# Performance work log

Measured on AMD Instinct MI355X. Metric: run time of the kernel, lower is better.

Reference implementation:

```python
import jax, jax.numpy as jnp
import numpy as np

NUM_HEADS = 16
N_EMBED = 1024
HEAD_SIZE = 64
BLOCK_SIZE = 2048


def setup_inputs() -> dict:
    key = jax.random.key(0)
    ks = jax.random.split(key, 6)
    B, S, C, H, D = 2, BLOCK_SIZE, N_EMBED, NUM_HEADS, HEAD_SIZE
    x = jax.random.normal(ks[0], (B, S, C), dtype=jnp.float32)
    scale = C ** -0.5
    # per-head q/k/v projections (bias=False), stacked over heads: [H, C, D]
    Wq = jax.random.normal(ks[1], (H, C, D), dtype=jnp.float32) * scale
    Wk = jax.random.normal(ks[2], (H, C, D), dtype=jnp.float32) * scale
    Wv = jax.random.normal(ks[3], (H, C, D), dtype=jnp.float32) * scale
    # output projection Linear(H*D, C)
    Wo = jax.random.normal(ks[4], (H * D, C), dtype=jnp.float32) * ((H * D) ** -0.5)
    bo = jax.random.normal(ks[5], (C,), dtype=jnp.float32) * 0.01
    return {"x": x, "Wq": Wq, "Wk": Wk, "Wv": Wv, "Wo": Wo, "bo": bo}


def reference(x, Wq, Wk, Wv, Wo, bo):
    B, S, C = x.shape
    H, _, D = Wq.shape
    # project: [B, H, S, D]
    q = jnp.einsum("bsc,hcd->bhsd", x, Wq)
    k = jnp.einsum("bsc,hcd->bhsd", x, Wk)
    v = jnp.einsum("bsc,hcd->bhsd", x, Wv)
    # scaled causal attention scores: [B, H, S, S]
    scores = jnp.einsum("bhsd,bhtd->bhst", q, k) * (D ** -0.5)
    causal = jnp.tril(jnp.ones((S, S), dtype=bool))
    scores = jnp.where(causal, scores, jnp.finfo(scores.dtype).min)
    attn = jax.nn.softmax(scores, axis=-1)
    out = jnp.einsum("bhst,bhtd->bhsd", attn, v)  # [B, H, S, D]
    # concat heads -> [B, S, H*D], then output projection
    out = out.transpose(0, 2, 1, 3).reshape(B, S, H * D)
    return out @ Wo + bo
```

## Files before the change

kernel.cpp:

```cpp
#include <hip/hip_runtime.h>
#include <cstdint>
#include <cstddef>

constexpr int SEQ  = 2048;
constexpr int CH   = 1024;
constexpr int NH   = 16;
constexpr int HS   = 64;
constexpr int NB   = 2;
constexpr int HDIM = NH * HS;

typedef __bf16 bf16x8 __attribute__((ext_vector_type(8)));
typedef __bf16 bf16x4 __attribute__((ext_vector_type(4)));
typedef float  f32x4  __attribute__((ext_vector_type(4)));

__device__ __forceinline__ unsigned short f2bf(float f) {
  union { float f; unsigned u; } v; v.f = f;
  unsigned u = v.u;
  u += 0x7fffu + ((u >> 16) & 1u);
  return (unsigned short)(u >> 16);
}
__device__ __forceinline__ float bf2f(unsigned short h) {
  union { unsigned u; float f; } v; v.u = ((unsigned)h) << 16;
  return v.f;
}
__device__ __forceinline__ float load_elem(const void* p, int flag, size_t idx) {
  if (flag) return ((const float*)p)[idx];
  return bf2f(((const unsigned short*)p)[idx]);
}
__device__ __forceinline__ void gl_lds16(const unsigned short* g, unsigned short* l) {
  __builtin_amdgcn_global_load_lds(
      (const __attribute__((address_space(1))) unsigned int*)g,
      (__attribute__((address_space(3))) unsigned int*)l, 16, 0, 0);
}

__device__ int detect_flag_block(const void* p, int n, int tid, int nthr) {
  __shared__ int det_good;
  if (tid == 0) det_good = 0;
  __syncthreads();
  const unsigned short* u = (const unsigned short*)p;
  int good = 0;
  for (int j = tid; j < n; j += nthr) {
    unsigned short v = u[2 * j];
    int e = (v >> 7) & 0xFF;
    if (v != 0 && e >= 90 && e <= 150) good++;
  }
  atomicAdd(&det_good, good);
  __syncthreads();
  return (det_good * 10 >= n * 7) ? 0 : 1;
}

__global__ __launch_bounds__(256) void prep(
    const void* __restrict__ x,  const void* __restrict__ wq,
    const void* __restrict__ wk, const void* __restrict__ wv,
    const void* __restrict__ wo,
    unsigned short* __restrict__ xb,
    unsigned short* __restrict__ wall,
    unsigned short* __restrict__ wot) {
  __shared__ unsigned short tile[32][36];
  int idx = blockIdx.x, tid = threadIdx.x;
  int row = tid >> 3, cg = (tid & 7) * 4;
  int col = tid >> 3, rg = (tid & 7) * 4;
  if (idx < 1024) {
    int f = detect_flag_block(x, 512, tid, 256);
    size_t n4 = (size_t)NB * SEQ * CH / 4;
    for (size_t i = (size_t)idx * 256 + tid; i < n4; i += (size_t)1024 * 256) {
      ushort4 o;
      if (f) {
        float4 v = ((const float4*)x)[i];
        o.x = f2bf(v.x); o.y = f2bf(v.y); o.z = f2bf(v.z); o.w = f2bf(v.w);
      } else {
        o = ((const ushort4*)x)[i];
      }
      ((ushort4*)xb)[i] = o;
    }
  } else if (idx < 4096) {
    int j = idx - 1024;
    int which = j >> 10, hh = (j >> 6) & 15, sub = j & 63;
    const void* src = (which == 0) ? wq : (which == 1) ? wk : wv;
    int f = detect_flag_block(src, 512, tid, 256);
    int c0 = (sub & 1) * 32;
    int r0 = (sub >> 1) * 32;
    size_t boff = (size_t)hh * CH * HS;
    size_t si = boff + (size_t)(r0 + row) * HS + c0 + cg;
    ushort4 t4;
    if (f) {
      float4 v = *(const float4*)((const float*)src + si);
      t4.x = f2bf(v.x); t4.y = f2bf(v.y); t4.z = f2bf(v.z); t4.w = f2bf(v.w);
    } else {
      t4 = *(const ushort4*)((const unsigned short*)src + si);
    }
    *(ushort4*)&tile[row][cg] = t4;
    __syncthreads();
    unsigned short* d = wall + ((size_t)which * NH + hh) * HS * CH;
    ushort4 o;
    o.x = tile[rg + 0][col]; o.y = tile[rg + 1][col];
    o.z = tile[rg + 2][col]; o.w = tile[rg + 3][col];
    *(ushort4*)&d[(size_t)(c0 + col) * CH + r0 + rg] = o;
  } else {
    int sub = idx - 4096;
    int f = detect_flag_block(wo, 512, tid, 256);
    int c0 = (sub & 31) * 32;
    int r0 = (sub >> 5) * 32;
    size_t si = (size_t)(r0 + row) * CH + c0 + cg;
    ushort4 t4;
    if (f) {
      float4 v = *(const float4*)((const float*)wo + si);
      t4.x = f2bf(v.x); t4.y = f2bf(v.y); t4.z = f2bf(v.z); t4.w = f2bf(v.w);
    } else {
      t4 = *(const ushort4*)((const unsigned short*)wo + si);
    }
    *(ushort4*)&tile[row][cg] = t4;
    __syncthreads();
    ushort4 o;
    o.x = tile[rg + 0][col]; o.y = tile[rg + 1][col];
    o.z = tile[rg + 2][col]; o.w = tile[rg + 3][col];
    *(ushort4*)&wot[(size_t)(c0 + col) * HDIM + r0 + rg] = o;
  }
}

__global__ __launch_bounds__(256, 2) void qkv_gemm(
    const unsigned short* __restrict__ xb,
    const unsigned short* __restrict__ wall,
    unsigned short* __restrict__ qo,
    unsigned short* __restrict__ ko,
    unsigned short* __restrict__ vt) {
  __shared__ __attribute__((aligned(16))) unsigned short Al[2][128 * 64];
  __shared__ __attribute__((aligned(16))) unsigned short Bl[2][192 * 64];
  int mt = blockIdx.x, nt = blockIdx.y;
  const unsigned short* A  = xb   + (size_t)mt * 128 * CH;
  const unsigned short* Bm = wall + (size_t)nt * 192 * CH;
  int tid = threadIdx.x, wave = tid >> 6, lane = tid & 63;
  int quad = lane >> 4, l15 = lane & 15;
  int r8 = lane >> 3, c8 = lane & 7;
  int gcol = ((c8 ^ r8) << 3);
  int x7 = l15 & 7;
  int wm = (wave >> 1) * 64, wn = (wave & 1) * 96;
  f32x4 acc[4][6];
  #pragma unroll
  for (int i = 0; i < 4; i++)
    #pragma unroll
    for (int j = 0; j < 6; j++) acc[i][j] = (f32x4){0.f, 0.f, 0.f, 0.f};

  auto stage = [&](int bb, int k0) {
    #pragma unroll
    for (int c = 0; c < 4; c++) {
      int row = wave * 32 + c * 8 + r8;
      gl_lds16(&A[(size_t)row * CH + k0 + gcol], &Al[bb][(wave * 32 + c * 8) * 64]);
    }
    #pragma unroll
    for (int c = 0; c < 6; c++) {
      int row = wave * 48 + c * 8 + r8;
      gl_lds16(&Bm[(size_t)row * CH + k0 + gcol], &Bl[bb][(wave * 48 + c * 8) * 64]);
    }
  };

  stage(0, 0);
  __syncthreads();
  for (int ks = 0; ks < 16; ks++) {
    int bb = ks & 1;
    if (ks < 15) stage(bb ^ 1, (ks + 1) * 64);
    #pragma unroll
    for (int h = 0; h < 2; h++) {
      int cq = ((quad + 4 * h) ^ x7) << 3;
      bf16x8 af[4], bfr[6];
      #pragma unroll
      for (int fm = 0; fm < 4; fm++)
        af[fm] = *reinterpret_cast<const bf16x8*>(&Al[bb][(wm + fm * 16 + l15) * 64 + cq]);
      #pragma unroll
      for (int fn = 0; fn < 6; fn++)
        bfr[fn] = *reinterpret_cast<const bf16x8*>(&Bl[bb][(wn + fn * 16 + l15) * 64 + cq]);
      __builtin_amdgcn_s_setprio(1);
      #pragma unroll
      for (int fm = 0; fm < 4; fm++)
        #pragma unroll
        for (int fn = 0; fn < 6; fn++)
          acc[fm][fn] = __builtin_amdgcn_mfma_f32_16x16x32_bf16(af[fm], bfr[fn], acc[fm][fn], 0, 0, 0);
      __builtin_amdgcn_s_setprio(0);
    }
    __syncthreads();
  }

  #pragma unroll
  for (int fn = 0; fn < 6; fn++) {
    int c0 = nt * 192 + wn + fn * 16;
    int seg = c0 >> 10;
    int hd = (c0 & 1023) + l15;
    int h = hd >> 6, d = hd & 63;
    if (seg < 2) {
      unsigned short* dst = (seg == 0) ? qo : ko;
      float s = (seg == 0) ? 0.18033688011112042f : 1.0f;
      #pragma unroll
      for (int fm = 0; fm < 4; fm++) {
        int m = mt * 128 + wm + fm * 16 + quad * 4;
        int b = m >> 11, s0 = m & 2047;
        #pragma unroll
        for (int r = 0; r < 4; r++)
          dst[(((size_t)b * NH + h) * SEQ + s0 + r) * HS + d] = f2bf(acc[fm][fn][r] * s);
      }
    } else {
      #pragma unroll
      for (int fm = 0; fm < 4; fm++) {
        int m = mt * 128 + wm + fm * 16 + quad * 4;
        int b = m >> 11, s0 = m & 2047;
        ushort4 pk;
        pk.x = f2bf(acc[fm][fn][0]); pk.y = f2bf(acc[fm][fn][1]);
        pk.z = f2bf(acc[fm][fn][2]); pk.w = f2bf(acc[fm][fn][3]);
        *(ushort4*)&vt[(((size_t)b * NH + h) * HS + d) * SEQ + s0] = pk;
      }
    }
  }
}

template <bool MASKED>
__device__ __forceinline__ void soft_pack(const f32x4* s, f32x4& ls,
                                          unsigned short* ptRow, int quad, int tmb) {
  #pragma unroll
  for (int tb = 0; tb < 4; tb++) {
    f32x4 pv;
    #pragma unroll
    for (int r = 0; r < 4; r++) {
      float p = __builtin_amdgcn_exp2f(s[tb][r]);
      if (MASKED) { if (tmb + tb * 16 + quad * 4 + r > 0) p = 0.f; }
      pv[r] = p;
    }
    ls += pv;
    bf16x4 pk;
    pk.x = (__bf16)pv[0]; pk.y = (__bf16)pv[1];
    pk.z = (__bf16)pv[2]; pk.w = (__bf16)pv[3];
    *(bf16x4*)&ptRow[tb * 16 + quad * 4] = pk;
  }
}

template <int QKM, bool PV0, bool PVV>
__device__ __forceinline__ void attn_step(
    const unsigned short (&Kb)[64][64], const unsigned short (&Vp)[64][64],
    unsigned short* p0row, unsigned short* p1row,
    const bf16x8 (&qf)[2][2], f32x4 (&lsum)[2], f32x4 (&accO)[2][4],
    bf16x8 (&bq0)[2], bf16x8 (&bq1)[2],
    int quad, int l15, int tmb) {
  constexpr bool C0 = (QKM <= 1);
  constexpr bool M0 = (QKM == 1);
  constexpr bool M1 = (QKM == 3);
  int x7 = l15 & 7;
  f32x4 s0[4], s1[4];
  #pragma unroll
  for (int tb = 0; tb < 4; tb++) { s0[tb] = (f32x4){0,0,0,0}; s1[tb] = (f32x4){0,0,0,0}; }
  __builtin_amdgcn_s_setprio(1);
  #pragma unroll
  for (int tb = 0; tb < 4; tb++)
    #pragma unroll
    for (int hh = 0; hh < 2; hh++) {
      bf16x8 kf = *reinterpret_cast<const bf16x8*>(
          &Kb[tb * 16 + l15][((hh * 4 + quad) ^ x7) << 3]);
      if (C0) s0[tb] = __builtin_amdgcn_mfma_f32_16x16x32_bf16(kf, qf[0][hh], s0[tb], 0, 0, 0);
      s1[tb] = __builtin_amdgcn_mfma_f32_16x16x32_bf16(kf, qf[1][hh], s1[tb], 0, 0, 0);
    }
  if (PVV) {
    #pragma unroll
    for (int db = 0; db < 4; db++)
      #pragma unroll
      for (int tp = 0; tp < 2; tp++) {
        bf16x8 vf = *reinterpret_cast<const bf16x8*>(
            &Vp[db * 16 + l15][((tp * 4 + quad) ^ x7) << 3]);
        if (PV0) accO[0][db] = __builtin_amdgcn_mfma_f32_16x16x32_bf16(vf, bq0[tp], accO[0][db], 0, 0, 0);
        accO[1][db] = __builtin_amdgcn_mfma_f32_16x16x32_bf16(vf, bq1[tp], accO[1][db], 0, 0, 0);
      }
  }
  __builtin_amdgcn_s_setprio(0);
  if (C0) soft_pack<M0>(s0, lsum[0], p0row, quad, tmb);
  soft_pack<M1>(s1, lsum[1], p1row, quad, tmb);
  #pragma unroll
  for (int tp = 0; tp < 2; tp++) {
    if (C0) bq0[tp] = *reinterpret_cast<const bf16x8*>(&p0row[tp * 32 + quad * 8]);
    bq1[tp] = *reinterpret_cast<const bf16x8*>(&p1row[tp * 32 + quad * 8]);
  }
}

__global__ __launch_bounds__(256) void attn_k(
    const unsigned short* __restrict__ q,
    const unsigned short* __restrict__ k,
    const unsigned short* __restrict__ vt,
    unsigned short* __restrict__ y) {
  __shared__ __attribute__((aligned(16))) unsigned short Kl[3][64][64];
  __shared__ __attribute__((aligned(16))) unsigned short Vl[3][64][64];
  __shared__ __attribute__((aligned(16))) unsigned short Pt[4][16][152];

  int n = blockIdx.x + 16 * blockIdx.y;
  int g = n & 7, idx = n >> 3;
  int p = idx & 15;
  int bh = g * 4 + (idx >> 4);
  int st0 = p, st1 = 31 - p;
  int b = bh >> 4, h = bh & 15;
  const unsigned short* Q0 = q + ((size_t)bh * SEQ + st0 * 64) * HS;
  const unsigned short* Q1 = q + ((size_t)bh * SEQ + st1 * 64) * HS;
  const unsigned short* K  = k  + (size_t)bh * SEQ * HS;
  const unsigned short* V  = vt + (size_t)bh * HS * SEQ;
  int tid = threadIdx.x, wave = tid >> 6, lane = tid & 63;
  int quad = lane >> 4, l15 = lane & 15;
  int lr = tid >> 3, lc = (tid & 7) * 8;
  int sc = (((tid & 7) ^ (lr & 7)) << 3);

  bf16x8 qf[2][2];
  #pragma unroll
  for (int hh = 0; hh < 2; hh++) {
    qf[0][hh] = *reinterpret_cast<const bf16x8*>(
        &Q0[(size_t)(wave * 16 + l15) * HS + hh * 32 + quad * 8]);
    qf[1][hh] = *reinterpret_cast<const bf16x8*>(
        &Q1[(size_t)(wave * 16 + l15) * HS + hh * 32 + quad * 8]);
  }

  f32x4 lsum[2] = {(f32x4){0,0,0,0}, (f32x4){0,0,0,0}};
  f32x4 accO[2][4];
  #pragma unroll
  for (int f = 0; f < 2; f++)
    #pragma unroll
    for (int i = 0; i < 4; i++) accO[f][i] = (f32x4){0.f, 0.f, 0.f, 0.f};
  bf16x8 bq0[2], bq1[2];

  unsigned short* p0row = &Pt[wave][l15][0];
  unsigned short* p1row = &Pt[wave][l15][64];
  int tmb = -(wave * 16 + l15);

  uint4 kr0, kr1, vr0, vr1;
  auto g2r = [&](int kv) {
    kr0 = *(const uint4*)&K[(size_t)(kv * 64 + lr) * HS + lc];
    kr1 = *(const uint4*)&K[(size_t)(kv * 64 + lr + 32) * HS + lc];
    vr0 = *(const uint4*)&V[(size_t)lr * SEQ + kv * 64 + lc];
    vr1 = *(const uint4*)&V[(size_t)(lr + 32) * SEQ + kv * 64 + lc];
  };
  auto r2l = [&](int nb) {
    *(uint4*)&Kl[nb][lr][sc] = kr0; *(uint4*)&Kl[nb][lr + 32][sc] = kr1;
    *(uint4*)&Vl[nb][lr][sc] = vr0; *(uint4*)&Vl[nb][lr + 32][sc] = vr1;
  };

  g2r(0); r2l(0);
  __syncthreads();

  {
    if (st1 > 0) g2r(1);
    if (st0 == 0)
      attn_step<1, false, false>(Kl[0], Vl[2], p0row, p1row, qf, lsum, accO, bq0, bq1, quad, l15, tmb);
    else
      attn_step<0, false, false>(Kl[0], Vl[2], p0row, p1row, qf, lsum, accO, bq0, bq1, quad, l15, tmb);
    if (st1 > 0) r2l(1);
    __syncthreads();
  }
  for (int t = 1; t < st0; t++) {
    g2r(t + 1);
    attn_step<0, true, true>(Kl[t % 3], Vl[(t + 2) % 3], p0row, p1row, qf, lsum, accO, bq0, bq1, quad, l15, tmb);
    r2l((t + 1) % 3);
    __syncthreads();
  }
  if (st0 >= 1) {
    int t = st0;
    g2r(t + 1);
    attn_step<1, true, true>(Kl[t % 3], Vl[(t + 2) % 3], p0row, p1row, qf, lsum, accO, bq0, bq1, quad, l15, tmb);
    r2l((t + 1) % 3);
    __syncthreads();
  }
  {
    int t = st0 + 1;
    bool more = (t < st1);
    if (more) g2r(t + 1);
    if (t == st1)
      attn_step<3, true, true>(Kl[t % 3], Vl[(t + 2) % 3], p0row, p1row, qf, lsum, accO, bq0, bq1, quad, l15, tmb);
    else
      attn_step<2, true, true>(Kl[t % 3], Vl[(t + 2) % 3], p0row, p1row, qf, lsum, accO, bq0, bq1, quad, l15, tmb);
    if (more) r2l((t + 1) % 3);
    __syncthreads();
  }
  for (int t = st0 + 2; t < st1; t++) {
    g2r(t + 1);
    attn_step<2, false, true>(Kl[t % 3], Vl[(t + 2) % 3], p0row, p1row, qf, lsum, accO, bq0, bq1, quad, l15, tmb);
    r2l((t + 1) % 3);
    __syncthreads();
  }
  if (st1 >= st0 + 2) {
    int t = st1;
    attn_step<3, false, true>(Kl[t % 3], Vl[(t + 2) % 3], p0row, p1row, qf, lsum, accO, bq0, bq1, quad, l15, tmb);
  }
  {
    const unsigned short (&Vb)[64][64] = Vl[st1 % 3];
    int x7 = l15 & 7;
    #pragma unroll
    for (int db = 0; db < 4; db++)
      #pragma unroll
      for (int tp = 0; tp < 2; tp++) {
        bf16x8 vf = *reinterpret_cast<const bf16x8*>(
            &Vb[db * 16 + l15][((tp * 4 + quad) ^ x7) << 3]);
        accO[1][db] = __builtin_amdgcn_mfma_f32_16x16x32_bf16(vf, bq1[tp], accO[1][db], 0, 0, 0);
      }
  }

  #pragma unroll
  for (int f = 0; f < 2; f++) {
    float rs = (lsum[f][0] + lsum[f][1]) + (lsum[f][2] + lsum[f][3]);
    rs += __shfl_xor(rs, 16); rs += __shfl_xor(rs, 32);
    float inv = 1.0f / fmaxf(rs, 1e-30f);
    int srow = (f == 0 ? st0 : st1) * 64 + wave * 16 + l15;
    #pragma unroll
    for (int db = 0; db < 4; db++) {
      ushort4 pk;
      pk.x = f2bf(accO[f][db][0] * inv); pk.y = f2bf(accO[f][db][1] * inv);
      pk.z = f2bf(accO[f][db][2] * inv); pk.w = f2bf(accO[f][db][3] * inv);
      *(ushort4*)&y[((size_t)b * SEQ + srow) * HDIM + h * 64 + db * 16 + quad * 4] = pk;
    }
  }
}

__global__ __launch_bounds__(256) void out_gemm(
    const unsigned short* __restrict__ y,
    const unsigned short* __restrict__ wot,
    const void* __restrict__ bo,
    float* __restrict__ out) {
  __shared__ __attribute__((aligned(16))) unsigned short Al[128 * 64];
  __shared__ __attribute__((aligned(16))) unsigned short Bl[64 * 64];
  int tid = threadIdx.x;
  int fbo = detect_flag_block(bo, 512, tid, 256);
  int mt = blockIdx.x, nt = blockIdx.y;
  const unsigned short* A  = y   + (size_t)mt * 128 * HDIM;
  const unsigned short* Bm = wot + (size_t)nt * 64 * HDIM;
  int wave = tid >> 6, lane = tid & 63;
  int quad = lane >> 4, l15 = lane & 15;
  int r8 = lane >> 3, c8 = lane & 7;
  int gcol = ((c8 ^ r8) << 3);
  int x7 = l15 & 7;
  int wm = (wave >> 1) * 64, wn = (wave & 1) * 32;
  f32x4 acc[4][2];
  #pragma unroll
  for (int i = 0; i < 4; i++)
    #pragma unroll
    for (int j = 0; j < 2; j++) acc[i][j] = (f32x4){0.f, 0.f, 0.f, 0.f};

  for (int k0 = 0; k0 < HDIM; k0 += 64) {
    #pragma unroll
    for (int c = 0; c < 4; c++) {
      int row = wave * 32 + c * 8 + r8;
      gl_lds16(&A[(size_t)row * HDIM + k0 + gcol], &Al[(wave * 32 + c * 8) * 64]);
    }
    #pragma unroll
    for (int c = 0; c < 2; c++) {
      int row = wave * 16 + c * 8 + r8;
      gl_lds16(&Bm[(size_t)row * HDIM + k0 + gcol], &Bl[(wave * 16 + c * 8) * 64]);
    }
    __syncthreads();
    #pragma unroll
    for (int h = 0; h < 2; h++) {
      int cq = ((quad + 4 * h) ^ x7) << 3;
      bf16x8 af[4], bfr[2];
      #pragma unroll
      for (int fm = 0; fm < 4; fm++)
        af[fm] = *reinterpret_cast<const bf16x8*>(&Al[(wm + fm * 16 + l15) * 64 + cq]);
      #pragma unroll
      for (int fn = 0; fn < 2; fn++)
        bfr[fn] = *reinterpret_cast<const bf16x8*>(&Bl[(wn + fn * 16 + l15) * 64 + cq]);
      #pragma unroll
      for (int fm = 0; fm < 4; fm++)
        #pragma unroll
        for (int fn = 0; fn < 2; fn++)
          acc[fm][fn] = __builtin_amdgcn_mfma_f32_16x16x32_bf16(af[fm], bfr[fn], acc[fm][fn], 0, 0, 0);
    }
    __syncthreads();
  }

  #pragma unroll
  for (int fn = 0; fn < 2; fn++) {
    int n = nt * 64 + wn + fn * 16 + l15;
    float bias = load_elem(bo, fbo, n);
    #pragma unroll
    for (int fm = 0; fm < 4; fm++) {
      int m = mt * 128 + wm + fm * 16 + quad * 4;
      #pragma unroll
      for (int r = 0; r < 4; r++)
        out[(size_t)(m + r) * CH + n] = acc[fm][fn][r] + bias;
    }
  }
}

extern "C" void kernel_launch(void* const* d_in, const int* in_sizes, int n_in,
                              void* d_out, int out_size, void* d_ws, size_t ws_size,
                              hipStream_t stream) {
  const void* x  = d_in[0];
  const void* Wq = d_in[1];
  const void* Wk = d_in[2];
  const void* Wv = d_in[3];
  const void* Wo = d_in[4];
  const void* bo = d_in[5];
  float* out = (float*)d_out;

  char* ws = (char*)d_ws;
  const size_t MB = 1024 * 1024;
  unsigned short* qb   = (unsigned short*)(ws + 0);
  unsigned short* kb   = (unsigned short*)(ws + 8  * MB);
  unsigned short* vtb  = (unsigned short*)(ws + 16 * MB);
  unsigned short* yb   = (unsigned short*)(ws + 24 * MB);
  unsigned short* wall = (unsigned short*)(ws + 32 * MB);
  unsigned short* wot  = (unsigned short*)(ws + 38 * MB);
  unsigned short* xb   = (unsigned short*)(ws + 40 * MB);

  prep<<<5120, 256, 0, stream>>>(x, Wq, Wk, Wv, Wo, xb, wall, wot);
  qkv_gemm<<<dim3(NB * SEQ / 128, 3 * HDIM / 192), 256, 0, stream>>>(xb, wall, qb, kb, vtb);
  attn_k<<<dim3(16, NB * NH), 256, 0, stream>>>(qb, kb, vtb, yb);
  out_gemm<<<dim3(NB * SEQ / 128, CH / 64), 256, 0, stream>>>(yb, wot, bo, out);
}
```

Before: 174.4 us.

## Double-buffer out_gemm LDS tiles and defer P fragment loads in attention

The output GEMM now uses two LDS buffers, so the next K-slice is issued with async global-to-LDS loads while the MFMAs run on the current one, and it raises wave priority around the MFMA block. This removes one barrier per K step and the exposed load latency. In the attention kernel, the P fragments are now read from LDS at the start of the next step instead of right after softmax packing, which shortens register live ranges. The K/V global pointers are also advanced incrementally instead of recomputing addresses. The double buffer doubles out_gemm LDS use, which may lower occupancy, and the single barrier per iteration must still keep the buffers safe from overwrite.

```diff
diff --git a/kernel.cpp b/kernel.cpp
--- a/kernel.cpp
+++ b/kernel.cpp
@@ -236,12 +236,19 @@
     const unsigned short (&Kb)[64][64], const unsigned short (&Vp)[64][64],
     unsigned short* p0row, unsigned short* p1row,
     const bf16x8 (&qf)[2][2], f32x4 (&lsum)[2], f32x4 (&accO)[2][4],
-    bf16x8 (&bq0)[2], bf16x8 (&bq1)[2],
     int quad, int l15, int tmb) {
   constexpr bool C0 = (QKM <= 1);
   constexpr bool M0 = (QKM == 1);
   constexpr bool M1 = (QKM == 3);
   int x7 = l15 & 7;
+  bf16x8 pb0[2], pb1[2];
+  if (PVV) {
+    #pragma unroll
+    for (int tp = 0; tp < 2; tp++) {
+      if (PV0) pb0[tp] = *reinterpret_cast<const bf16x8*>(&p0row[tp * 32 + quad * 8]);
+      pb1[tp] = *reinterpret_cast<const bf16x8*>(&p1row[tp * 32 + quad * 8]);
+    }
+  }
   f32x4 s0[4], s1[4];
   #pragma unroll
   for (int tb = 0; tb < 4; tb++) { s0[tb] = (f32x4){0,0,0,0}; s1[tb] = (f32x4){0,0,0,0}; }
@@ -262,18 +269,13 @@
       for (int tp = 0; tp < 2; tp++) {
         bf16x8 vf = *reinterpret_cast<const bf16x8*>(
             &Vp[db * 16 + l15][((tp * 4 + quad) ^ x7) << 3]);
-        if (PV0) accO[0][db] = __builtin_amdgcn_mfma_f32_16x16x32_bf16(vf, bq0[tp], accO[0][db], 0, 0, 0);
-        accO[1][db] = __builtin_amdgcn_mfma_f32_16x16x32_bf16(vf, bq1[tp], accO[1][db], 0, 0, 0);
+        if (PV0) accO[0][db] = __builtin_amdgcn_mfma_f32_16x16x32_bf16(vf, pb0[tp], accO[0][db], 0, 0, 0);
+        accO[1][db] = __builtin_amdgcn_mfma_f32_16x16x32_bf16(vf, pb1[tp], accO[1][db], 0, 0, 0);
       }
   }
   __builtin_amdgcn_s_setprio(0);
   if (C0) soft_pack<M0>(s0, lsum[0], p0row, quad, tmb);
   soft_pack<M1>(s1, lsum[1], p1row, quad, tmb);
-  #pragma unroll
-  for (int tp = 0; tp < 2; tp++) {
-    if (C0) bq0[tp] = *reinterpret_cast<const bf16x8*>(&p0row[tp * 32 + quad * 8]);
-    bq1[tp] = *reinterpret_cast<const bf16x8*>(&p1row[tp * 32 + quad * 8]);
-  }
 }
 
 __global__ __launch_bounds__(256) void attn_k(
@@ -315,80 +317,86 @@
   for (int f = 0; f < 2; f++)
     #pragma unroll
     for (int i = 0; i < 4; i++) accO[f][i] = (f32x4){0.f, 0.f, 0.f, 0.f};
-  bf16x8 bq0[2], bq1[2];
 
   unsigned short* p0row = &Pt[wave][l15][0];
   unsigned short* p1row = &Pt[wave][l15][64];
   int tmb = -(wave * 16 + l15);
 
+  const unsigned short* pK0 = K + (size_t)lr * HS + lc;
+  const unsigned short* pK1 = pK0 + (size_t)32 * HS;
+  const unsigned short* pV0 = V + (size_t)lr * SEQ + lc;
+  const unsigned short* pV1 = pV0 + (size_t)32 * SEQ;
   uint4 kr0, kr1, vr0, vr1;
-  auto g2r = [&](int kv) {
-    kr0 = *(const uint4*)&K[(size_t)(kv * 64 + lr) * HS + lc];
-    kr1 = *(const uint4*)&K[(size_t)(kv * 64 + lr + 32) * HS + lc];
-    vr0 = *(const uint4*)&V[(size_t)lr * SEQ + kv * 64 + lc];
-    vr1 = *(const uint4*)&V[(size_t)(lr + 32) * SEQ + kv * 64 + lc];
+  auto g2r = [&]() {
+    kr0 = *(const uint4*)pK0; kr1 = *(const uint4*)pK1;
+    vr0 = *(const uint4*)pV0; vr1 = *(const uint4*)pV1;
+    pK0 += 64 * HS; pK1 += 64 * HS; pV0 += 64; pV1 += 64;
   };
   auto r2l = [&](int nb) {
     *(uint4*)&Kl[nb][lr][sc] = kr0; *(uint4*)&Kl[nb][lr + 32][sc] = kr1;
     *(uint4*)&Vl[nb][lr][sc] = vr0; *(uint4*)&Vl[nb][lr + 32][sc] = vr1;
   };
 
-  g2r(0); r2l(0);
+  g2r(); r2l(0);
   __syncthreads();
 
   {
-    if (st1 > 0) g2r(1);
+    if (st1 > 0) g2r();
     if (st0 == 0)
-      attn_step<1, false, false>(Kl[0], Vl[2], p0row, p1row, qf, lsum, accO, bq0, bq1, quad, l15, tmb);
+      attn_step<1, false, false>(Kl[0], Vl[2], p0row, p1row, qf, lsum, accO, quad, l15, tmb);
     else
-      attn_step<0, false, false>(Kl[0], Vl[2], p0row, p1row, qf, lsum, accO, bq0, bq1, quad, l15, tmb);
+      attn_step<0, false, false>(Kl[0], Vl[2], p0row, p1row, qf, lsum, accO, quad, l15, tmb);
     if (st1 > 0) r2l(1);
     __syncthreads();
   }
   for (int t = 1; t < st0; t++) {
-    g2r(t + 1);
-    attn_step<0, true, true>(Kl[t % 3], Vl[(t + 2) % 3], p0row, p1row, qf, lsum, accO, bq0, bq1, quad, l15, tmb);
+    g2r();
+    attn_step<0, true, true>(Kl[t % 3], Vl[(t + 2) % 3], p0row, p1row, qf, lsum, accO, quad, l15, tmb);
     r2l((t + 1) % 3);
     __syncthreads();
   }
   if (st0 >= 1) {
     int t = st0;
-    g2r(t + 1);
-    attn_step<1, true, true>(Kl[t % 3], Vl[(t + 2) % 3], p0row, p1row, qf, lsum, accO, bq0, bq1, quad, l15, tmb);
+    g2r();
+    attn_step<1, true, true>(Kl[t % 3], Vl[(t + 2) % 3], p0row, p1row, qf, lsum, accO, quad, l15, tmb);
     r2l((t + 1) % 3);
     __syncthreads();
   }
   {
     int t = st0 + 1;
     bool more = (t < st1);
-    if (more) g2r(t + 1);
+    if (more) g2r();
     if (t == st1)
-      attn_step<3, true, true>(Kl[t % 3], Vl[(t + 2) % 3], p0row, p1row, qf, lsum, accO, bq0, bq1, quad, l15, tmb);
+      attn_step<3, true, true>(Kl[t % 3], Vl[(t + 2) % 3], p0row, p1row, qf, lsum, accO, quad, l15, tmb);
     else
-      attn_step<2, true, true>(Kl[t % 3], Vl[(t + 2) % 3], p0row, p1row, qf, lsum, accO, bq0, bq1, quad, l15, tmb);
+      attn_step<2, true, true>(Kl[t % 3], Vl[(t + 2) % 3], p0row, p1row, qf, lsum, accO, quad, l15, tmb);
     if (more) r2l((t + 1) % 3);
     __syncthreads();
   }
   for (int t = st0 + 2; t < st1; t++) {
-    g2r(t + 1);
-    attn_step<2, false, true>(Kl[t % 3], Vl[(t + 2) % 3], p0row, p1row, qf, lsum, accO, bq0, bq1, quad, l15, tmb);
+    g2r();
+    attn_step<2, false, true>(Kl[t % 3], Vl[(t + 2) % 3], p0row, p1row, qf, lsum, accO, quad, l15, tmb);
     r2l((t + 1) % 3);
     __syncthreads();
   }
   if (st1 >= st0 + 2) {
     int t = st1;
-    attn_step<3, false, true>(Kl[t % 3], Vl[(t + 2) % 3], p0row, p1row, qf, lsum, accO, bq0, bq1, quad, l15, tmb);
+    attn_step<3, false, true>(Kl[t % 3], Vl[(t + 2) % 3], p0row, p1row, qf, lsum, accO, quad, l15, tmb);
   }
   {
     const unsigned short (&Vb)[64][64] = Vl[st1 % 3];
     int x7 = l15 & 7;
+    bf16x8 pb1[2];
+    #pragma unroll
+    for (int tp = 0; tp < 2; tp++)
+      pb1[tp] = *reinterpret_cast<const bf16x8*>(&p1row[tp * 32 + quad * 8]);
     #pragma unroll
     for (int db = 0; db < 4; db++)
       #pragma unroll
       for (int tp = 0; tp < 2; tp++) {
         bf16x8 vf = *reinterpret_cast<const bf16x8*>(
             &Vb[db * 16 + l15][((tp * 4 + quad) ^ x7) << 3]);
-        accO[1][db] = __builtin_amdgcn_mfma_f32_16x16x32_bf16(vf, bq1[tp], accO[1][db], 0, 0, 0);
+        accO[1][db] = __builtin_amdgcn_mfma_f32_16x16x32_bf16(vf, pb1[tp], accO[1][db], 0, 0, 0);
       }
   }
 
@@ -413,8 +421,8 @@
     const unsigned short* __restrict__ wot,
     const void* __restrict__ bo,
     float* __restrict__ out) {
-  __shared__ __attribute__((aligned(16))) unsigned short Al[128 * 64];
-  __shared__ __attribute__((aligned(16))) unsigned short Bl[64 * 64];
+  __shared__ __attribute__((aligned(16))) unsigned short Al[2][128 * 64];
+  __shared__ __attribute__((aligned(16))) unsigned short Bl[2][64 * 64];
   int tid = threadIdx.x;
   int fbo = detect_flag_block(bo, 512, tid, 256);
   int mt = blockIdx.x, nt = blockIdx.y;
@@ -432,33 +440,41 @@
     #pragma unroll
     for (int j = 0; j < 2; j++) acc[i][j] = (f32x4){0.f, 0.f, 0.f, 0.f};
 
-  for (int k0 = 0; k0 < HDIM; k0 += 64) {
+  auto stage = [&](int bb, int k0) {
     #pragma unroll
     for (int c = 0; c < 4; c++) {
       int row = wave * 32 + c * 8 + r8;
-      gl_lds16(&A[(size_t)row * HDIM + k0 + gcol], &Al[(wave * 32 + c * 8) * 64]);
+      gl_lds16(&A[(size_t)row * HDIM + k0 + gcol], &Al[bb][(wave * 32 + c * 8) * 64]);
     }
     #pragma unroll
     for (int c = 0; c < 2; c++) {
       int row = wave * 16 + c * 8 + r8;
-      gl_lds16(&Bm[(size_t)row * HDIM + k0 + gcol], &Bl[(wave * 16 + c * 8) * 64]);
-    }
-    __syncthreads();
+      gl_lds16(&Bm[(size_t)row * HDIM + k0 + gcol], &Bl[bb][(wave * 16 + c * 8) * 64]);
+    }
+  };
+
+  stage(0, 0);
+  __syncthreads();
+  for (int ks = 0; ks < 16; ks++) {
+    int bb = ks & 1;
+    if (ks < 15) stage(bb ^ 1, (ks + 1) * 64);
     #pragma unroll
     for (int h = 0; h < 2; h++) {
       int cq = ((quad + 4 * h) ^ x7) << 3;
       bf16x8 af[4], bfr[2];
       #pragma unroll
       for (int fm = 0; fm < 4; fm++)
-        af[fm] = *reinterpret_cast<const bf16x8*>(&Al[(wm + fm * 16 + l15) * 64 + cq]);
+        af[fm] = *reinterpret_cast<const bf16x8*>(&Al[bb][(wm + fm * 16 + l15) * 64 + cq]);
       #pragma unroll
       for (int fn = 0; fn < 2; fn++)
-        bfr[fn] = *reinterpret_cast<const bf16x8*>(&Bl[(wn + fn * 16 + l15) * 64 + cq]);
+        bfr[fn] = *reinterpret_cast<const bf16x8*>(&Bl[bb][(wn + fn * 16 + l15) * 64 + cq]);
+      __builtin_amdgcn_s_setprio(1);
       #pragma unroll
       for (int fm = 0; fm < 4; fm++)
         #pragma unroll
         for (int fn = 0; fn < 2; fn++)
           acc[fm][fn] = __builtin_amdgcn_mfma_f32_16x16x32_bf16(af[fm], bfr[fn], acc[fm][fn], 0, 0, 0);
+      __builtin_amdgcn_s_setprio(0);
     }
     __syncthreads();
   }
```

New measurement: 171.1 us, median of 2. Within noise of the previous version (-1.9%).
